# Performance work log

Measured on AMD Instinct MI355X. Metric: run time of the kernel, lower is better.

## Reference

```python
import jax, jax.numpy as jnp
import numpy as np

CELL_SIDE = 1.0
N_CELL = 4          # self.n
POOL = 8            # pool_size
HIDDEN = 128        # hidden_dim == pooling_dim for type_='social'
GRID = N_CELL * POOL  # 32
N_AGENTS = 1024


def setup_inputs() -> dict:
    key = jax.random.key(0)
    k1, k2, k3, k4, k5 = jax.random.split(key, 5)
    hidden_state = jax.random.normal(k1, (N_AGENTS, HIDDEN), jnp.float32)
    obs1 = jax.random.normal(k2, (N_AGENTS, 2), jnp.float32)
    obs2 = jax.random.normal(k3, (N_AGENTS, 2), jnp.float32)
    fan_in = N_CELL * N_CELL * HIDDEN  # 2048
    W = jax.random.normal(k4, (HIDDEN, fan_in), jnp.float32) / np.float32(np.sqrt(fan_in))
    b = jax.random.normal(k5, (HIDDEN,), jnp.float32) * 0.01
    return {"hidden_state": hidden_state, "obs1": obs1, "obs2": obs2, "W": W, "b": b}


def _social_grid(hidden_state, obs2):
    """Vectorized equivalent of Pooling.social: for each agent i, scatter the
    hidden states of in-range other agents into a 32x32 sub-grid, then 8x8
    sum-pool (lp_pool2d with p=1) down to 4x4."""
    N = obs2.shape[0]
    D = hidden_state.shape[1]
    # relative position of agent j in agent i's fine grid: (N, N, 2)
    rel = (obs2[None, :, :] - obs2[:, None, :]) / (CELL_SIDE / POOL) + GRID / 2.0
    valid = ~jnp.eye(N, dtype=bool)                       # one_cold: exclude self
    nan_x = jnp.isnan(obs2[:, 0])
    valid &= ~nan_x[None, :]                              # other agent NaN mask
    valid &= ~nan_x[:, None]                              # self NaN -> zero grid
    valid &= jnp.all((rel >= 0) & (rel < GRID), axis=-1)  # range mask
    oij = jnp.where(valid[..., None], rel, 0.0).astype(jnp.int32)  # trunc == .long()
    # flat cell index; invalid pairs go to a dump slot GRID*GRID
    oi = jnp.where(valid, oij[..., 0] * GRID + oij[..., 1], GRID * GRID)
    vals = jnp.broadcast_to(hidden_state[None, :, :], (N, N, D))

    def scatter(idx, v):
        # occ[oi] = other_values  (set semantics, as in torch fancy assignment)
        return jnp.zeros((GRID * GRID + 1, D), v.dtype).at[idx].set(v)[: GRID * GRID]

    occ = jax.vmap(scatter)(oi, vals)  # (N, GRID*GRID, D)
    # torch: occ.view(1, -1, 32, 32) reinterprets the (1024, D) buffer as (D, 32, 32)
    occ = occ.reshape(N, D, N_CELL, POOL, N_CELL, POOL).sum(axis=(3, 5))  # sum-pool 8x8
    return occ.reshape(N, D * N_CELL * N_CELL)  # (N, 2048)


def reference(hidden_state, obs1, obs2, W, b):
    grid = _social_grid(hidden_state, obs2)
    return grid @ W.T + b  # embedding Linear(2048 -> 128)
```

## Files before the change

### kernel.cpp

```cpp
#include <hip/hip_runtime.h>
#include <math.h>

#define N_AGENTS 1024
#define HIDDEN   128
#define GRIDSZ   32
#define NCELLS   1024
#define KDIM     2048

typedef __attribute__((ext_vector_type(8))) short short8;
typedef __attribute__((ext_vector_type(4))) float floatx4;

static __device__ __forceinline__ ushort f2bf(float x) {
    union { float f; unsigned u; } v; v.f = x;
    return (ushort)((v.u + 0x7fffu + ((v.u >> 16) & 1u)) >> 16);
}

__global__ __launch_bounds__(512, 2) void k_fused(
        const float* __restrict__ hidden, const float* __restrict__ obs2,
        const float* __restrict__ W, const float* __restrict__ bias,
        float* __restrict__ out) {
    __shared__ float2 spos[N_AGENTS];
    __shared__ float4 ssh[N_AGENTS];
    __shared__ int win[16][NCELLS];
    __shared__ __align__(16) ushort Gs[256 * 16 * 8];

    const int tid = threadIdx.x;
    const int mt = blockIdx.x >> 2;
    const int ng = blockIdx.x & 3;
    const int ibase = mt * 16;

    const float2* o2 = (const float2*)obs2;
    spos[tid] = o2[tid];
    spos[tid + 512] = o2[tid + 512];
#pragma unroll
    for (int q = 0; q < 8; ++q) {
        int idx = q * 512 + tid;
        int j = idx >> 2, c = idx & 3;
        const float* h = hidden + j * HIDDEN + c * 8;
        float s = 0.f;
#pragma unroll
        for (int u = 0; u < 4; ++u) {
            float4 a = *(const float4*)(h + u * 32);
            float4 b = *(const float4*)(h + u * 32 + 4);
            s += a.x + a.y + a.z + a.w + b.x + b.y + b.z + b.w;
        }
        ((float*)&ssh[j])[c] = s;
    }
    {
        int* wl = &win[0][0];
#pragma unroll
        for (int q = 0; q < 32; ++q) wl[q * 512 + tid] = -1;
    }
    __syncthreads();

    float2 pi[16];
#pragma unroll
    for (int a = 0; a < 16; ++a) pi[a] = spos[ibase + a];
#pragma unroll
    for (int half = 0; half < 2; ++half) {
        int jj = half * 512 + tid;
        float2 pj = spos[jj];
        if (!isnan(pj.x)) {
#pragma unroll
            for (int a = 0; a < 16; ++a) {
                if (jj == ibase + a) continue;
                float rx = (pj.x - pi[a].x) * 8.0f + 16.0f;
                float ry = (pj.y - pi[a].y) * 8.0f + 16.0f;
                if (rx >= 0.f && rx < 32.f && ry >= 0.f && ry < 32.f)
                    atomicMax(&win[a][(int)rx * GRIDSZ + (int)ry], jj);
            }
        }
    }
    __syncthreads();

#pragma unroll
    for (int q = 0; q < 16; ++q) {
        int task = q * 512 + tid;
        int a = task & 15, p = task >> 4;
        int w0 = win[a][2 * p], w1 = win[a][2 * p + 1];
        float4 v = {0.f, 0.f, 0.f, 0.f};
        if (w0 >= 0) { float4 s = ssh[w0]; v.x += s.x; v.y += s.y; v.z += s.z; v.w += s.w; }
        if (w1 >= 0) { float4 s = ssh[w1]; v.x += s.x; v.y += s.y; v.z += s.z; v.w += s.w; }
        ushort4 u;
        u.x = f2bf(v.x); u.y = f2bf(v.y); u.z = f2bf(v.z); u.w = f2bf(v.w);
        *(ushort4*)(Gs + ((p >> 1) * 16 + a) * 8 + (p & 1) * 4) = u;
    }
    __syncthreads();

    const int wv = tid >> 6, lane = tid & 63;
    const int ntl = wv >> 2, ks = wv & 3;
    const int r16 = lane & 15, quad = lane >> 4;
    const int col = ng * 32 + ntl * 16 + r16;
    const float* Wp = W + (size_t)col * KDIM + ks * 512 + quad * 8;
    floatx4 acc = {0.f, 0.f, 0.f, 0.f};
#pragma unroll
    for (int kb = 0; kb < 16; ++kb) {
        short8 av = *(const short8*)(Gs + ((ks * 64 + kb * 4 + quad) * 16 + r16) * 8);
        float4 wa = *(const float4*)(Wp + kb * 32);
        float4 wb = *(const float4*)(Wp + kb * 32 + 4);
        short8 bv;
        bv[0] = (short)f2bf(wa.x); bv[1] = (short)f2bf(wa.y);
        bv[2] = (short)f2bf(wa.z); bv[3] = (short)f2bf(wa.w);
        bv[4] = (short)f2bf(wb.x); bv[5] = (short)f2bf(wb.y);
        bv[6] = (short)f2bf(wb.z); bv[7] = (short)f2bf(wb.w);
        acc = __builtin_amdgcn_mfma_f32_16x16x32_bf16(av, bv, acc, 0, 0, 0);
    }

    float* pbuf = (float*)&win[0][0];
    *(floatx4*)&pbuf[tid * 4] = acc;
    __syncthreads();
    if (ks == 0) {
#pragma unroll
        for (int ksi = 1; ksi < 4; ++ksi) {
            floatx4 pv = *(const floatx4*)&pbuf[((wv + ksi) * 64 + lane) * 4];
            acc[0] += pv[0]; acc[1] += pv[1]; acc[2] += pv[2]; acc[3] += pv[3];
        }
        float bc = bias[col];
#pragma unroll
        for (int r = 0; r < 4; ++r)
            out[(size_t)(ibase + quad * 4 + r) * HIDDEN + col] = acc[r] + bc;
    }
}

extern "C" void kernel_launch(void* const* d_in, const int* in_sizes, int n_in,
                              void* d_out, int out_size, void* d_ws, size_t ws_size,
                              hipStream_t stream) {
    const float* hidden = (const float*)d_in[0];
    const float* obs2   = (const float*)d_in[2];
    const float* W      = (const float*)d_in[3];
    const float* b      = (const float*)d_in[4];
    float* out = (float*)d_out;
    (void)d_ws; (void)ws_size;

    k_fused<<<256, 512, 0, stream>>>(hidden, obs2, W, b, out);
}
```

Before: 80.34 us.

## Split hidden-sum and W bf16 conversion into a separate prep kernel

Measured after the change: 75.08 us. -6.6%, faster.

```diff
diff --git a/kernel.cpp b/kernel.cpp
--- a/kernel.cpp
+++ b/kernel.cpp
@@ -15,9 +15,34 @@
     return (ushort)((v.u + 0x7fffu + ((v.u >> 16) & 1u)) >> 16);
 }
 
-__global__ __launch_bounds__(512, 2) void k_fused(
-        const float* __restrict__ hidden, const float* __restrict__ obs2,
-        const float* __restrict__ W, const float* __restrict__ bias,
+__global__ __launch_bounds__(256) void k_prep(const float* __restrict__ hidden,
+                                              const float* __restrict__ W,
+                                              float* __restrict__ Sh,
+                                              ushort* __restrict__ Wb) {
+    int gt = blockIdx.x * 256 + threadIdx.x;
+    {
+        float4 w = ((const float4*)W)[gt];
+        ushort4 u;
+        u.x = f2bf(w.x); u.y = f2bf(w.y); u.z = f2bf(w.z); u.w = f2bf(w.w);
+        *(ushort4*)(Wb + (size_t)gt * 4) = u;
+    }
+    if (gt < N_AGENTS * 4) {
+        int j = gt >> 2, c = gt & 3;
+        const float* h = hidden + j * HIDDEN + c * 8;
+        float s = 0.f;
+#pragma unroll
+        for (int u = 0; u < 4; ++u) {
+            float4 a = *(const float4*)(h + u * 32);
+            float4 b = *(const float4*)(h + u * 32 + 4);
+            s += a.x + a.y + a.z + a.w + b.x + b.y + b.z + b.w;
+        }
+        Sh[gt] = s;
+    }
+}
+
+__global__ __launch_bounds__(512, 2) void k_main(
+        const float* __restrict__ obs2, const float4* __restrict__ Sh4,
+        const ushort* __restrict__ Wb, const float* __restrict__ bias,
         float* __restrict__ out) {
     __shared__ float2 spos[N_AGENTS];
     __shared__ float4 ssh[N_AGENTS];
@@ -32,24 +57,13 @@
     const float2* o2 = (const float2*)obs2;
     spos[tid] = o2[tid];
     spos[tid + 512] = o2[tid + 512];
+    ssh[tid] = Sh4[tid];
+    ssh[tid + 512] = Sh4[tid + 512];
+    {
+        int4* wl = (int4*)&win[0][0];
+        int4 m1 = {-1, -1, -1, -1};
 #pragma unroll
-    for (int q = 0; q < 8; ++q) {
-        int idx = q * 512 + tid;
-        int j = idx >> 2, c = idx & 3;
-        const float* h = hidden + j * HIDDEN + c * 8;
-        float s = 0.f;
-#pragma unroll
-        for (int u = 0; u < 4; ++u) {
-            float4 a = *(const float4*)(h + u * 32);
-            float4 b = *(const float4*)(h + u * 32 + 4);
-            s += a.x + a.y + a.z + a.w + b.x + b.y + b.z + b.w;
-        }
-        ((float*)&ssh[j])[c] = s;
-    }
-    {
-        int* wl = &win[0][0];
-#pragma unroll
-        for (int q = 0; q < 32; ++q) wl[q * 512 + tid] = -1;
+        for (int q = 0; q < 8; ++q) wl[q * 512 + tid] = m1;
     }
     __syncthreads();
 
@@ -91,21 +105,16 @@
     const int ntl = wv >> 2, ks = wv & 3;
     const int r16 = lane & 15, quad = lane >> 4;
     const int col = ng * 32 + ntl * 16 + r16;
-    const float* Wp = W + (size_t)col * KDIM + ks * 512 + quad * 8;
+    const ushort* Wp = Wb + (size_t)col * KDIM + ks * 512 + quad * 8;
     floatx4 acc = {0.f, 0.f, 0.f, 0.f};
 #pragma unroll
     for (int kb = 0; kb < 16; ++kb) {
         short8 av = *(const short8*)(Gs + ((ks * 64 + kb * 4 + quad) * 16 + r16) * 8);
-        float4 wa = *(const float4*)(Wp + kb * 32);
-        float4 wb = *(const float4*)(Wp + kb * 32 + 4);
-        short8 bv;
-        bv[0] = (short)f2bf(wa.x); bv[1] = (short)f2bf(wa.y);
-        bv[2] = (short)f2bf(wa.z); bv[3] = (short)f2bf(wa.w);
-        bv[4] = (short)f2bf(wb.x); bv[5] = (short)f2bf(wb.y);
-        bv[6] = (short)f2bf(wb.z); bv[7] = (short)f2bf(wb.w);
+        short8 bv = *(const short8*)(Wp + kb * 32);
         acc = __builtin_amdgcn_mfma_f32_16x16x32_bf16(av, bv, acc, 0, 0, 0);
     }
 
+    __syncthreads();
     float* pbuf = (float*)&win[0][0];
     *(floatx4*)&pbuf[tid * 4] = acc;
     __syncthreads();
@@ -130,7 +139,10 @@
     const float* W      = (const float*)d_in[3];
     const float* b      = (const float*)d_in[4];
     float* out = (float*)d_out;
-    (void)d_ws; (void)ws_size;
 
-    k_fused<<<256, 512, 0, stream>>>(hidden, obs2, W, b, out);
+    float*  Sh = (float*) d_ws;
+    ushort* Wb = (ushort*)((char*)d_ws + 65536);
+
+    k_prep<<<256, 256, 0, stream>>>(hidden, W, Sh, Wb);
+    k_main<<<256, 512, 0, stream>>>(obs2, (const float4*)Sh, Wb, b, out);
 }
```
